# Kernel optimization log

Hardware: AMD Instinct MI355X
Metric: run time of the kernel (lower is better)

The kernel has to match this reference:

```python
import jax, jax.numpy as jnp
import numpy as np

BLOCK = 64
KH = 8        # num_k_head
G = 4         # gqa_group_size
D = 128       # model_hidden_size (head dim)
DG = 128      # gate_hidden_size
EPS = 1e-6
BSZ = 4
MAXS = 4096
LENGTHS = np.array([4096, 3584, 3072, 4096])


def rotate_half(x):
    h = x.shape[-1] // 2
    return jnp.concatenate([-x[..., h:], x[..., :h]], axis=-1)


def rmsnorm(x, w):
    x32 = x.astype(jnp.float32)
    y = x32 * jax.lax.rsqrt(jnp.mean(x32 * x32, axis=-1, keepdims=True) + EPS)
    return (y * w).astype(x.dtype)


def _rope_tables(n_pos, dim):
    inv = 1.0 / (10000.0 ** (np.arange(0, dim, 2, dtype=np.float32) / dim))
    ang = np.arange(n_pos, dtype=np.float32)[:, None] * inv[None, :]
    emb = np.concatenate([ang, ang], axis=-1)
    return np.cos(emb), np.sin(emb)


def setup_inputs() -> dict:
    key = jax.random.key(0)
    k1, k2, k3, k4, k5, k6 = jax.random.split(key, 6)
    total = int(LENGTHS.sum())
    cu = np.concatenate([[0], np.cumsum(LENGTHS)]).astype(np.int32)
    unpad_idx = np.concatenate([b * MAXS + np.arange(L) for b, L in enumerate(LENGTHS)]).astype(np.int64)
    # block-causal + validity mask (bool), shape (BSZ, 1, MAXS, MAXS//BLOCK)
    nb = MAXS // BLOCK
    qpos = np.arange(MAXS)
    bidx = np.arange(nb)
    causal = (qpos[:, None] // BLOCK) >= bidx[None, :]
    qvalid = qpos[None, :] < LENGTHS[:, None]
    bvalid = (bidx * BLOCK)[None, :] < LENGTHS[:, None]
    mask = causal[None] & qvalid[:, :, None] & bvalid[:, None, :]
    cos_q, sin_q = _rope_tables(MAXS, DG)
    cos_k, sin_k = _rope_tables(nb, DG)
    xavq = float(np.sqrt(6.0 / (D + DG)))
    xavk = float(np.sqrt(6.0 / (2 * D + DG)))
    return {
        "q": jax.random.normal(k1, (total, KH * G, D), jnp.float32),
        "k": jax.random.normal(k2, (total, KH, D), jnp.float32),
        "wq": jax.random.uniform(k3, (KH, G, D, DG), jnp.float32, -xavq, xavq),
        "wk": jax.random.uniform(k4, (KH, 2 * D, DG), jnp.float32, -xavk, xavk),
        "qnorm_w": jnp.ones((DG,), jnp.float32),
        "knorm_w": jnp.ones((DG,), jnp.float32),
        "cos_q": jnp.tile(jnp.asarray(cos_q)[None], (BSZ, 1, 1)),
        "sin_q": jnp.tile(jnp.asarray(sin_q)[None], (BSZ, 1, 1)),
        "cos_k": jnp.tile(jnp.asarray(cos_k)[None], (BSZ, 1, 1)),
        "sin_k": jnp.tile(jnp.asarray(sin_k)[None], (BSZ, 1, 1)),
        "attention_mask": jnp.asarray(mask)[:, None, :, :],
        "cu_seqlens": jnp.asarray(cu),
        "unpad_indices": jnp.asarray(unpad_idx),
        "max_seqlen": MAXS,
    }


def reference(q, k, wq, wk, qnorm_w, knorm_w, cos_q, sin_q, cos_k, sin_k,
              attention_mask, cu_seqlens, unpad_indices, max_seqlen):
    T = q.shape[0]
    bsz = cu_seqlens.shape[0] - 1
    nb = max_seqlen // BLOCK
    lengths = cu_seqlens[1:] - cu_seqlens[:-1]

    # --- Q path: per-group head-pooling projection (HeadPoolingLinear, Qproj) ---
    qp = jnp.einsum('skgi,kgio->sko', q.reshape(T, KH, G, D), wq)  # (T, KH, DG)
    qpad = jnp.zeros((bsz * max_seqlen, KH, DG), q.dtype).at[unpad_indices].set(qp)
    qpad = qpad.reshape(bsz, max_seqlen, KH, DG).transpose(0, 2, 1, 3)  # (b, KH, S, DG)
    qpad = rmsnorm(qpad, qnorm_w)
    qpad = qpad * cos_q[:, None] + rotate_half(qpad) * sin_q[:, None]

    # --- K path: pad, block max+avg pool (masked for varlen), project ---
    kpad = jnp.zeros((bsz * max_seqlen, KH, D), k.dtype).at[unpad_indices].set(k)
    kpad = kpad.reshape(bsz, nb, BLOCK, KH, D)
    pos = jnp.arange(max_seqlen).reshape(nb, BLOCK)
    valid = pos[None] < lengths[:, None, None]          # (b, nb, BLOCK)
    v = valid[..., None, None]                          # (b, nb, BLOCK, 1, 1)
    cnt = valid.sum(-1)[..., None, None]                # (b, nb, 1, 1)
    kmax = jnp.where(v, kpad, -jnp.inf).max(axis=2)
    kmax = jnp.where(cnt > 0, kmax, 0.0)
    kavg = jnp.where(v, kpad, 0.0).sum(axis=2) / jnp.maximum(cnt, 1).astype(k.dtype)
    kcat = jnp.concatenate([kmax, kavg], axis=-1)       # (b, nb, KH, 2D)
    kk = jnp.einsum('bhsi,hio->bhso', kcat.transpose(0, 2, 1, 3), wk)  # (b, KH, nb, DG)
    kk = rmsnorm(kk, knorm_w)
    kk = kk * cos_k[:, None] + rotate_half(kk) * sin_k[:, None]

    # --- QK gate scores ---
    attn = jnp.einsum('bhsd,bhtd->bhst', qpad, kk) * (1.0 / np.sqrt(DG))
    return jnp.where(attention_mask, attn, -1e20)
```

## Files before the change

kernel.cpp:

```cpp
#include <hip/hip_runtime.h>
#include <cstdint>
#include <cstddef>

#define BSZ   4
#define MAXS  4096
#define NB    64
#define KH    8
#define DH    128
#define DG    128
#define KHGD  4096
#define GD    512

typedef __attribute__((ext_vector_type(8))) short  short8;
typedef __attribute__((ext_vector_type(4))) float  f32x4;

static __device__ __forceinline__ unsigned bf16hi_bits(float x) {
    unsigned u = __float_as_uint(x);
    return (u + 0x7FFFu + ((u >> 16) & 1u)) & 0xFFFF0000u;
}
static __device__ __forceinline__ unsigned short bf16_rne(float x) {
    unsigned u = __float_as_uint(x);
    return (unsigned short)((u + 0x7FFFu + ((u >> 16) & 1u)) >> 16);
}

__global__ __launch_bounds__(256)
void prep_wq(const float* __restrict__ wq, unsigned short* __restrict__ Bp)
{
    const int wid  = blockIdx.x * 4 + (threadIdx.x >> 6);
    const int lane = threadIdx.x & 63;
    const int h  = wid >> 7, kt = (wid >> 4) & 7, kf = (wid >> 3) & 1, cf = wid & 7;
    const int n  = cf * 16 + (lane & 15);
    const int k0 = kt * 64 + kf * 32 + (lane >> 4) * 8;

    short8 hi, lo;
#pragma unroll
    for (int j = 0; j < 8; ++j) {
        const float x = wq[(size_t)(h * GD + k0 + j) * DG + n];
        const unsigned hb = bf16hi_bits(x);
        hi[j] = (short)(hb >> 16);
        lo[j] = (short)bf16_rne(x - __uint_as_float(hb));
    }
    unsigned short* p = Bp + (size_t)wid * 1024 + lane * 8;
    *(short8*)p         = hi;
    *(short8*)(p + 512) = lo;
}

__global__ __launch_bounds__(64, 2)
void qproj_mfma(const float* __restrict__ q,
                const unsigned short* __restrict__ Bp,
                const float* __restrict__ qnw,
                const float* __restrict__ cosq,
                const float* __restrict__ sinq,
                const int*   __restrict__ cu,
                unsigned short* __restrict__ qh,
                unsigned short* __restrict__ ql,
                int T)
{
    const int lane = threadIdx.x;
    const int h    = blockIdx.x;
    const int row0 = blockIdx.y * 64;
    const int lr = lane & 15, lq = lane >> 4;

    f32x4 acc[4][8];
#pragma unroll
    for (int rf = 0; rf < 4; ++rf)
#pragma unroll
        for (int cf = 0; cf < 8; ++cf) acc[rf][cf] = (f32x4){0.f, 0.f, 0.f, 0.f};

    const float* qb = q + (size_t)h * GD + lq * 8;
    const float* aptr[4];
#pragma unroll
    for (int rf = 0; rf < 4; ++rf) {
        int grow = row0 + rf * 16 + lr;
        if (grow > T - 1) grow = T - 1;
        aptr[rf] = qb + (size_t)grow * KHGD;
    }

    for (int kt = 0; kt < 8; ++kt) {
        const int kb = kt * 64;
#pragma unroll
        for (int kf = 0; kf < 2; ++kf) {
            f32x4 a0[4], a1[4];
#pragma unroll
            for (int rf = 0; rf < 4; ++rf) {
                const float* p = aptr[rf] + kb + kf * 32;
                a0[rf] = *(const f32x4*)p;
                a1[rf] = *(const f32x4*)(p + 4);
            }
            short8 ah[4], al[4];
#pragma unroll
            for (int rf = 0; rf < 4; ++rf) {
#pragma unroll
                for (int j = 0; j < 4; ++j) {
                    float x = a0[rf][j];
                    unsigned hb = bf16hi_bits(x);
                    ah[rf][j] = (short)(hb >> 16);
                    al[rf][j] = (short)bf16_rne(x - __uint_as_float(hb));
                    float y = a1[rf][j];
                    unsigned hb2 = bf16hi_bits(y);
                    ah[rf][j + 4] = (short)(hb2 >> 16);
                    al[rf][j + 4] = (short)bf16_rne(y - __uint_as_float(hb2));
                }
            }
            const unsigned short* bp =
                Bp + (size_t)(((h * 8 + kt) * 2 + kf) * 8) * 1024 + lane * 8;
#pragma unroll
            for (int cf = 0; cf < 8; ++cf) {
                const short8 bh = *(const short8*)(bp + cf * 1024);
                const short8 bl = *(const short8*)(bp + cf * 1024 + 512);
#pragma unroll
                for (int rf = 0; rf < 4; ++rf) {
                    acc[rf][cf] = __builtin_amdgcn_mfma_f32_16x16x32_bf16(ah[rf], bh, acc[rf][cf], 0, 0, 0);
                    acc[rf][cf] = __builtin_amdgcn_mfma_f32_16x16x32_bf16(ah[rf], bl, acc[rf][cf], 0, 0, 0);
                    acc[rf][cf] = __builtin_amdgcn_mfma_f32_16x16x32_bf16(al[rf], bh, acc[rf][cf], 0, 0, 0);
                }
            }
        }
    }

    const int cu1 = cu[1], cu2 = cu[2], cu3 = cu[3];
    float wn[8];
#pragma unroll
    for (int cf = 0; cf < 8; ++cf) wn[cf] = qnw[cf * 16 + lr];

#pragma unroll
    for (int rf = 0; rf < 4; ++rf) {
#pragma unroll
        for (int r = 0; r < 4; ++r) {
            float vv[8];
            float ss = 0.f;
#pragma unroll
            for (int cf = 0; cf < 8; ++cf) { vv[cf] = acc[rf][cf][r]; ss += vv[cf] * vv[cf]; }
            ss += __shfl_xor(ss, 1);
            ss += __shfl_xor(ss, 2);
            ss += __shfl_xor(ss, 4);
            ss += __shfl_xor(ss, 8);
            const float rn = 1.0f / sqrtf(ss * (1.0f / 128.0f) + 1e-6f);

            const int t = row0 + rf * 16 + lq * 4 + r;
            if (t < T) {
                int b = 0, cub = 0;
                if (t >= cu1) { b = 1; cub = cu1; }
                if (t >= cu2) { b = 2; cub = cu2; }
                if (t >= cu3) { b = 3; cub = cu3; }
                const int s = t - cub;

                float y[8];
#pragma unroll
                for (int cf = 0; cf < 8; ++cf) y[cf] = vv[cf] * rn * wn[cf];

                const float* cb = cosq + ((size_t)b * MAXS + s) * DG + lr;
                const float* sb = sinq + ((size_t)b * MAXS + s) * DG + lr;
                unsigned short* oh = qh + ((size_t)t * KH + h) * DG + lr;
                unsigned short* ol = ql + ((size_t)t * KH + h) * DG + lr;
#pragma unroll
                for (int cf = 0; cf < 8; ++cf) {
                    const float rot = (cf < 4) ? -y[cf + 4] : y[cf - 4];
                    const float o = y[cf] * cb[cf * 16] + rot * sb[cf * 16];
                    const unsigned hb = bf16hi_bits(o);
                    oh[cf * 16] = (unsigned short)(hb >> 16);
                    ol[cf * 16] = bf16_rne(o - __uint_as_float(hb));
                }
            }
        }
    }
}

__global__ __launch_bounds__(256, 2)
void kproj_kernel(const float* __restrict__ k,
                  const float* __restrict__ wk,
                  const float* __restrict__ knw,
                  const float* __restrict__ cosk,
                  const float* __restrict__ sink,
                  const int*   __restrict__ cu,
                  unsigned short* __restrict__ krh,
                  unsigned short* __restrict__ krl)
{
    __shared__ float kcat[KH][2 * DH];

    const int tid = threadIdx.x;
    const int blk = blockIdx.x, b = blockIdx.y;
    const int lb = cu[b];
    const int L  = cu[b + 1] - lb;
    const int nv = min(64, L - blk * 64);
    if (nv <= 0) return;

    const float* kbase = k + (size_t)(lb + blk * 64) * (KH * DH) + tid * 4;
    float4 vmax = make_float4(-3.0e38f, -3.0e38f, -3.0e38f, -3.0e38f);
    float4 vsum = make_float4(0.f, 0.f, 0.f, 0.f);
#pragma unroll 4
    for (int j = 0; j < nv; ++j) {
        const float4 v = *(const float4*)(kbase + (size_t)j * (KH * DH));
        vmax.x = fmaxf(vmax.x, v.x); vmax.y = fmaxf(vmax.y, v.y);
        vmax.z = fmaxf(vmax.z, v.z); vmax.w = fmaxf(vmax.w, v.w);
        vsum.x += v.x; vsum.y += v.y; vsum.z += v.z; vsum.w += v.w;
    }
    {
        const float inv = 1.0f / (float)nv;
        const int hh = tid >> 5, dd = (tid & 31) * 4;
        *(float4*)&kcat[hh][dd] = vmax;
        const float4 va = make_float4(vsum.x * inv, vsum.y * inv, vsum.z * inv, vsum.w * inv);
        *(float4*)&kcat[hh][128 + dd] = va;
    }
    __syncthreads();

    const int h = tid >> 5, oc = tid & 31, o = oc * 4;
    float4 a4 = make_float4(0.f, 0.f, 0.f, 0.f);
    const float* wbb = wk + (size_t)h * (2 * DH) * DG + o;
#pragma unroll 8
    for (int kk = 0; kk < 2 * DH; ++kk) {
        const float a = kcat[h][kk];
        const float4 w = *(const float4*)(wbb + (size_t)kk * DG);
        a4.x += a * w.x; a4.y += a * w.y; a4.z += a * w.z; a4.w += a * w.w;
    }

    float ss = a4.x * a4.x + a4.y * a4.y + a4.z * a4.z + a4.w * a4.w;
    ss += __shfl_xor(ss, 1);
    ss += __shfl_xor(ss, 2);
    ss += __shfl_xor(ss, 4);
    ss += __shfl_xor(ss, 8);
    ss += __shfl_xor(ss, 16);
    const float r = 1.0f / sqrtf(ss * (1.0f / 128.0f) + 1e-6f);

    const float4 wn = *(const float4*)(knw + o);
    const float y0 = a4.x * r * wn.x;
    const float y1 = a4.y * r * wn.y;
    const float y2 = a4.z * r * wn.z;
    const float y3 = a4.w * r * wn.w;

    const float p0 = __shfl_xor(y0, 16);
    const float p1 = __shfl_xor(y1, 16);
    const float p2 = __shfl_xor(y2, 16);
    const float p3 = __shfl_xor(y3, 16);
    const float r0 = (oc < 16) ? -p0 : p0;
    const float r1 = (oc < 16) ? -p1 : p1;
    const float r2 = (oc < 16) ? -p2 : p2;
    const float r3 = (oc < 16) ? -p3 : p3;

    const float* cb = cosk + ((size_t)b * NB + blk) * DG + o;
    const float* sb = sink + ((size_t)b * NB + blk) * DG + o;
    const float4 c4 = *(const float4*)cb;
    const float4 s4 = *(const float4*)sb;

    float v[4];
    v[0] = y0 * c4.x + r0 * s4.x;
    v[1] = y1 * c4.y + r1 * s4.y;
    v[2] = y2 * c4.z + r2 * s4.z;
    v[3] = y3 * c4.w + r3 * s4.w;

    ushort4 sh, sl;
    unsigned hb;
    hb = bf16hi_bits(v[0]); sh.x = (unsigned short)(hb >> 16); sl.x = bf16_rne(v[0] - __uint_as_float(hb));
    hb = bf16hi_bits(v[1]); sh.y = (unsigned short)(hb >> 16); sl.y = bf16_rne(v[1] - __uint_as_float(hb));
    hb = bf16hi_bits(v[2]); sh.z = (unsigned short)(hb >> 16); sl.z = bf16_rne(v[2] - __uint_as_float(hb));
    hb = bf16hi_bits(v[3]); sh.w = (unsigned short)(hb >> 16); sl.w = bf16_rne(v[3] - __uint_as_float(hb));

    const size_t ko = (((size_t)b * KH + h) * NB + blk) * DG + o;
    *(ushort4*)(krh + ko) = sh;
    *(ushort4*)(krl + ko) = sl;
}

__global__ __launch_bounds__(256, 2)
void score_mfma(const unsigned short* __restrict__ qh,
                const unsigned short* __restrict__ ql,
                const unsigned short* __restrict__ krh,
                const unsigned short* __restrict__ krl,
                const int* __restrict__ cu,
                float* __restrict__ out, int T)
{
    const int tid = threadIdx.x;
    const int lane = tid & 63, wid = tid >> 6;
    const int c = blockIdx.x, h = blockIdx.y, b = blockIdx.z;
    const int L = cu[b + 1] - cu[b];
    float* ob = out + (((size_t)b * KH + h) * MAXS + c * 64) * NB;

    if (c * 64 >= L) {
        const f32x4 m4 = (f32x4){-1e20f, -1e20f, -1e20f, -1e20f};
#pragma unroll
        for (int i = 0; i < 4; ++i) ((f32x4*)ob)[tid + i * 256] = m4;
        return;
    }
    const int nt  = c + 1;
    const int ncf = (nt + 15) >> 4;
    const int lr = lane & 15, lq = lane >> 4;

    int qrow = cu[b] + c * 64 + wid * 16 + lr;
    if (qrow > T - 1) qrow = T - 1;
    const unsigned short* qhp = qh + ((size_t)qrow * KH + h) * DG + lq * 8;
    const unsigned short* qlp = ql + ((size_t)qrow * KH + h) * DG + lq * 8;
    const unsigned short* kbh = krh + (((size_t)b * KH + h) * NB + lr) * DG + lq * 8;
    const unsigned short* kbl = krl + (((size_t)b * KH + h) * NB + lr) * DG + lq * 8;

    f32x4 acc[4];
#pragma unroll
    for (int cf = 0; cf < 4; ++cf) acc[cf] = (f32x4){0.f, 0.f, 0.f, 0.f};

#pragma unroll
    for (int kf = 0; kf < 4; ++kf) {
        const short8 ah = *(const short8*)(qhp + kf * 32);
        const short8 al = *(const short8*)(qlp + kf * 32);
#pragma unroll
        for (int cf = 0; cf < 4; ++cf) {
            if (cf < ncf) {
                const short8 bh = *(const short8*)(kbh + cf * 2048 + kf * 32);
                const short8 bl = *(const short8*)(kbl + cf * 2048 + kf * 32);
                acc[cf] = __builtin_amdgcn_mfma_f32_16x16x32_bf16(ah, bh, acc[cf], 0, 0, 0);
                acc[cf] = __builtin_amdgcn_mfma_f32_16x16x32_bf16(ah, bl, acc[cf], 0, 0, 0);
                acc[cf] = __builtin_amdgcn_mfma_f32_16x16x32_bf16(al, bh, acc[cf], 0, 0, 0);
            }
        }
    }

    const float scale = 0.08838834764831845f;
#pragma unroll
    for (int cf = 0; cf < 4; ++cf) {
        const int t = cf * 16 + lr;
#pragma unroll
        for (int r = 0; r < 4; ++r) {
            const int srow = c * 64 + wid * 16 + lq * 4 + r;
            float v = (cf < ncf) ? acc[cf][r] * scale : -1e20f;
            v = (srow < L && t < nt) ? v : -1e20f;
            ob[(size_t)(wid * 16 + lq * 4 + r) * NB + t] = v;
        }
    }
}

extern "C" void kernel_launch(void* const* d_in, const int* in_sizes, int n_in,
                              void* d_out, int out_size, void* d_ws, size_t ws_size,
                              hipStream_t stream)
{
    const float* q    = (const float*)d_in[0];
    const float* k    = (const float*)d_in[1];
    const float* wq   = (const float*)d_in[2];
    const float* wk   = (const float*)d_in[3];
    const float* qnw  = (const float*)d_in[4];
    const float* knw  = (const float*)d_in[5];
    const float* cosq = (const float*)d_in[6];
    const float* sinq = (const float*)d_in[7];
    const float* cosk = (const float*)d_in[8];
    const float* sink = (const float*)d_in[9];
    const int*   cu   = (const int*)d_in[11];

    const int T = in_sizes[0] / KHGD;

    unsigned short* qh  = (unsigned short*)d_ws;
    unsigned short* ql  = qh  + (size_t)T * KH * DG;
    unsigned short* krh = ql  + (size_t)T * KH * DG;
    unsigned short* krl = krh + (size_t)BSZ * KH * NB * DG;
    unsigned short* Bp  = krl + (size_t)BSZ * KH * NB * DG;
    (void)ws_size; (void)n_in; (void)out_size;

    prep_wq<<<256, 256, 0, stream>>>(wq, Bp);
    kproj_kernel<<<dim3(NB, BSZ), 256, 0, stream>>>(k, wk, knw, cosk, sink, cu, krh, krl);
    qproj_mfma<<<dim3(KH, (T + 63) / 64), 64, 0, stream>>>(q, Bp, qnw, cosq, sinq, cu, qh, ql, T);
    score_mfma<<<dim3(NB, KH, BSZ), 256, 0, stream>>>(qh, ql, krh, krl, cu, (float*)d_out, T);
}
```

Measured before the change: 513.7 us.

## Fuse Q projection with gate score computation, staging rotated Q in LDS

Merges the Q projection/RMSNorm/RoPE kernel and the QK score kernel into one kernel per (batch, 64-row chunk, head). The normalized, rotated Q tile is staged through swizzled shared memory instead of being written to and re-read from global hi/lo bf16 buffers. This removes that intermediate global traffic and one launch. It also swaps MFMA operand roles so weights are the A operand, and uses truncation rather than round-to-nearest for the bf16 hi/lo split, which slightly changes numerics.

After: 516.0 us. Within noise of the previous version (+0.5%).

```diff
diff --git a/kernel.cpp b/kernel.cpp
--- a/kernel.cpp
+++ b/kernel.cpp
@@ -11,8 +11,12 @@
 #define KHGD  4096
 #define GD    512
 
-typedef __attribute__((ext_vector_type(8))) short  short8;
-typedef __attribute__((ext_vector_type(4))) float  f32x4;
+typedef __attribute__((ext_vector_type(8))) short        short8;
+typedef __attribute__((ext_vector_type(4))) float        f32x4;
+typedef __attribute__((ext_vector_type(4))) unsigned int u32x4;
+typedef __attribute__((ext_vector_type(2))) unsigned int u32x2;
+
+union frag16 { u32x4 u; short8 s; };
 
 static __device__ __forceinline__ unsigned bf16hi_bits(float x) {
     unsigned u = __float_as_uint(x);
@@ -21,6 +25,15 @@
 static __device__ __forceinline__ unsigned short bf16_rne(float x) {
     unsigned u = __float_as_uint(x);
     return (unsigned short)((u + 0x7FFFu + ((u >> 16) & 1u)) >> 16);
+}
+static __device__ __forceinline__ void split_pair(float x0, float x1,
+                                                  unsigned& hi, unsigned& lo) {
+    unsigned u0 = __float_as_uint(x0), u1 = __float_as_uint(x1);
+    unsigned h0 = u0 & 0xFFFF0000u, h1 = u1 & 0xFFFF0000u;
+    float r0 = x0 - __uint_as_float(h0);
+    float r1 = x1 - __uint_as_float(h1);
+    hi = (u0 >> 16) | h1;
+    lo = (__float_as_uint(r0) >> 16) | (__float_as_uint(r1) & 0xFFFF0000u);
 }
 
 __global__ __launch_bounds__(256)
@@ -28,9 +41,9 @@
 {
     const int wid  = blockIdx.x * 4 + (threadIdx.x >> 6);
     const int lane = threadIdx.x & 63;
-    const int h  = wid >> 7, kt = (wid >> 4) & 7, kf = (wid >> 3) & 1, cf = wid & 7;
-    const int n  = cf * 16 + (lane & 15);
-    const int k0 = kt * 64 + kf * 32 + (lane >> 4) * 8;
+    const int h  = wid >> 7, kf16 = (wid >> 3) & 15, of = wid & 7;
+    const int n  = of * 16 + (lane & 15);
+    const int k0 = kf16 * 32 + (lane >> 4) * 8;
 
     short8 hi, lo;
 #pragma unroll
@@ -43,127 +56,6 @@
     unsigned short* p = Bp + (size_t)wid * 1024 + lane * 8;
     *(short8*)p         = hi;
     *(short8*)(p + 512) = lo;
-}
-
-__global__ __launch_bounds__(64, 2)
-void qproj_mfma(const float* __restrict__ q,
-                const unsigned short* __restrict__ Bp,
-                const float* __restrict__ qnw,
-                const float* __restrict__ cosq,
-                const float* __restrict__ sinq,
-                const int*   __restrict__ cu,
-                unsigned short* __restrict__ qh,
-                unsigned short* __restrict__ ql,
-                int T)
-{
-    const int lane = threadIdx.x;
-    const int h    = blockIdx.x;
-    const int row0 = blockIdx.y * 64;
-    const int lr = lane & 15, lq = lane >> 4;
-
-    f32x4 acc[4][8];
-#pragma unroll
-    for (int rf = 0; rf < 4; ++rf)
-#pragma unroll
-        for (int cf = 0; cf < 8; ++cf) acc[rf][cf] = (f32x4){0.f, 0.f, 0.f, 0.f};
-
-    const float* qb = q + (size_t)h * GD + lq * 8;
-    const float* aptr[4];
-#pragma unroll
-    for (int rf = 0; rf < 4; ++rf) {
-        int grow = row0 + rf * 16 + lr;
-        if (grow > T - 1) grow = T - 1;
-        aptr[rf] = qb + (size_t)grow * KHGD;
-    }
-
-    for (int kt = 0; kt < 8; ++kt) {
-        const int kb = kt * 64;
-#pragma unroll
-        for (int kf = 0; kf < 2; ++kf) {
-            f32x4 a0[4], a1[4];
-#pragma unroll
-            for (int rf = 0; rf < 4; ++rf) {
-                const float* p = aptr[rf] + kb + kf * 32;
-                a0[rf] = *(const f32x4*)p;
-                a1[rf] = *(const f32x4*)(p + 4);
-            }
-            short8 ah[4], al[4];
-#pragma unroll
-            for (int rf = 0; rf < 4; ++rf) {
-#pragma unroll
-                for (int j = 0; j < 4; ++j) {
-                    float x = a0[rf][j];
-                    unsigned hb = bf16hi_bits(x);
-                    ah[rf][j] = (short)(hb >> 16);
-                    al[rf][j] = (short)bf16_rne(x - __uint_as_float(hb));
-                    float y = a1[rf][j];
-                    unsigned hb2 = bf16hi_bits(y);
-                    ah[rf][j + 4] = (short)(hb2 >> 16);
-                    al[rf][j + 4] = (short)bf16_rne(y - __uint_as_float(hb2));
-                }
-            }
-            const unsigned short* bp =
-                Bp + (size_t)(((h * 8 + kt) * 2 + kf) * 8) * 1024 + lane * 8;
-#pragma unroll
-            for (int cf = 0; cf < 8; ++cf) {
-                const short8 bh = *(const short8*)(bp + cf * 1024);
-                const short8 bl = *(const short8*)(bp + cf * 1024 + 512);
-#pragma unroll
-                for (int rf = 0; rf < 4; ++rf) {
-                    acc[rf][cf] = __builtin_amdgcn_mfma_f32_16x16x32_bf16(ah[rf], bh, acc[rf][cf], 0, 0, 0);
-                    acc[rf][cf] = __builtin_amdgcn_mfma_f32_16x16x32_bf16(ah[rf], bl, acc[rf][cf], 0, 0, 0);
-                    acc[rf][cf] = __builtin_amdgcn_mfma_f32_16x16x32_bf16(al[rf], bh, acc[rf][cf], 0, 0, 0);
-                }
-            }
-        }
-    }
-
-    const int cu1 = cu[1], cu2 = cu[2], cu3 = cu[3];
-    float wn[8];
-#pragma unroll
-    for (int cf = 0; cf < 8; ++cf) wn[cf] = qnw[cf * 16 + lr];
-
-#pragma unroll
-    for (int rf = 0; rf < 4; ++rf) {
-#pragma unroll
-        for (int r = 0; r < 4; ++r) {
-            float vv[8];
-            float ss = 0.f;
-#pragma unroll
-            for (int cf = 0; cf < 8; ++cf) { vv[cf] = acc[rf][cf][r]; ss += vv[cf] * vv[cf]; }
-            ss += __shfl_xor(ss, 1);
-            ss += __shfl_xor(ss, 2);
-            ss += __shfl_xor(ss, 4);
-            ss += __shfl_xor(ss, 8);
-            const float rn = 1.0f / sqrtf(ss * (1.0f / 128.0f) + 1e-6f);
-
-            const int t = row0 + rf * 16 + lq * 4 + r;
-            if (t < T) {
-                int b = 0, cub = 0;
-                if (t >= cu1) { b = 1; cub = cu1; }
-                if (t >= cu2) { b = 2; cub = cu2; }
-                if (t >= cu3) { b = 3; cub = cu3; }
-                const int s = t - cub;
-
-                float y[8];
-#pragma unroll
-                for (int cf = 0; cf < 8; ++cf) y[cf] = vv[cf] * rn * wn[cf];
-
-                const float* cb = cosq + ((size_t)b * MAXS + s) * DG + lr;
-                const float* sb = sinq + ((size_t)b * MAXS + s) * DG + lr;
-                unsigned short* oh = qh + ((size_t)t * KH + h) * DG + lr;
-                unsigned short* ol = ql + ((size_t)t * KH + h) * DG + lr;
-#pragma unroll
-                for (int cf = 0; cf < 8; ++cf) {
-                    const float rot = (cf < 4) ? -y[cf + 4] : y[cf - 4];
-                    const float o = y[cf] * cb[cf * 16] + rot * sb[cf * 16];
-                    const unsigned hb = bf16hi_bits(o);
-                    oh[cf * 16] = (unsigned short)(hb >> 16);
-                    ol[cf * 16] = bf16_rne(o - __uint_as_float(hb));
-                }
-            }
-        }
-    }
 }
 
 __global__ __launch_bounds__(256, 2)
@@ -260,67 +152,159 @@
     *(ushort4*)(krl + ko) = sl;
 }
 
-__global__ __launch_bounds__(256, 2)
-void score_mfma(const unsigned short* __restrict__ qh,
-                const unsigned short* __restrict__ ql,
-                const unsigned short* __restrict__ krh,
-                const unsigned short* __restrict__ krl,
-                const int* __restrict__ cu,
-                float* __restrict__ out, int T)
+__global__ __launch_bounds__(64, 2)
+void qscore_fused(const float* __restrict__ q,
+                  const unsigned short* __restrict__ Bp,
+                  const float* __restrict__ qnw,
+                  const float* __restrict__ cosq,
+                  const float* __restrict__ sinq,
+                  const unsigned short* __restrict__ krh,
+                  const unsigned short* __restrict__ krl,
+                  const int* __restrict__ cu,
+                  float* __restrict__ out)
 {
-    const int tid = threadIdx.x;
-    const int lane = tid & 63, wid = tid >> 6;
-    const int c = blockIdx.x, h = blockIdx.y, b = blockIdx.z;
-    const int L = cu[b + 1] - cu[b];
+    __shared__ unsigned short ldsh[2048];
+    __shared__ unsigned short ldsl[2048];
+
+    const int lane = threadIdx.x;
+    const int lq = lane >> 4, lr = lane & 15;
+    const int h = blockIdx.y;
+    const int b = blockIdx.x >> 6, c = blockIdx.x & 63;
+    const int lb = cu[b];
+    const int L  = cu[b + 1] - lb;
     float* ob = out + (((size_t)b * KH + h) * MAXS + c * 64) * NB;
 
     if (c * 64 >= L) {
-        const f32x4 m4 = (f32x4){-1e20f, -1e20f, -1e20f, -1e20f};
-#pragma unroll
-        for (int i = 0; i < 4; ++i) ((f32x4*)ob)[tid + i * 256] = m4;
+        const f32x4 m4 = {-1e20f, -1e20f, -1e20f, -1e20f};
+#pragma unroll
+        for (int i = 0; i < 16; ++i) ((f32x4*)ob)[lane + i * 64] = m4;
         return;
     }
+
+    f32x4 acc[8][4];
+#pragma unroll
+    for (int of = 0; of < 8; ++of)
+#pragma unroll
+        for (int sf = 0; sf < 4; ++sf) acc[of][sf] = (f32x4){0.f, 0.f, 0.f, 0.f};
+
+    const float* qbase = q + (size_t)(lb + c * 64) * KHGD + h * GD;
+    const unsigned short* bpb = Bp + (size_t)h * 16 * 8192 + lane * 8;
+
+#pragma unroll 2
+    for (int kf = 0; kf < 16; ++kf) {
+        frag16 bh[4], bl[4];
+#pragma unroll
+        for (int sf = 0; sf < 4; ++sf) {
+            const float* p = qbase + (size_t)(sf * 16 + lr) * KHGD + kf * 32 + lq * 8;
+            const f32x4 x0 = *(const f32x4*)p;
+            const f32x4 x1 = *(const f32x4*)(p + 4);
+            unsigned hw0, lw0, hw1, lw1, hw2, lw2, hw3, lw3;
+            split_pair(x0[0], x0[1], hw0, lw0);
+            split_pair(x0[2], x0[3], hw1, lw1);
+            split_pair(x1[0], x1[1], hw2, lw2);
+            split_pair(x1[2], x1[3], hw3, lw3);
+            bh[sf].u = (u32x4){hw0, hw1, hw2, hw3};
+            bl[sf].u = (u32x4){lw0, lw1, lw2, lw3};
+        }
+        const unsigned short* bpk = bpb + (size_t)kf * 8192;
+#pragma unroll
+        for (int of = 0; of < 8; ++of) {
+            const short8 ah = *(const short8*)(bpk + of * 1024);
+            const short8 al = *(const short8*)(bpk + of * 1024 + 512);
+#pragma unroll
+            for (int sf = 0; sf < 4; ++sf) {
+                acc[of][sf] = __builtin_amdgcn_mfma_f32_16x16x32_bf16(ah, bh[sf].s, acc[of][sf], 0, 0, 0);
+                acc[of][sf] = __builtin_amdgcn_mfma_f32_16x16x32_bf16(ah, bl[sf].s, acc[of][sf], 0, 0, 0);
+                acc[of][sf] = __builtin_amdgcn_mfma_f32_16x16x32_bf16(al, bh[sf].s, acc[of][sf], 0, 0, 0);
+            }
+        }
+    }
+
+    f32x4 wn4[8];
+#pragma unroll
+    for (int of = 0; of < 8; ++of)
+        wn4[of] = *(const f32x4*)(qnw + of * 16 + lq * 4);
+
     const int nt  = c + 1;
     const int ncf = (nt + 15) >> 4;
-    const int lr = lane & 15, lq = lane >> 4;
-
-    int qrow = cu[b] + c * 64 + wid * 16 + lr;
-    if (qrow > T - 1) qrow = T - 1;
-    const unsigned short* qhp = qh + ((size_t)qrow * KH + h) * DG + lq * 8;
-    const unsigned short* qlp = ql + ((size_t)qrow * KH + h) * DG + lq * 8;
-    const unsigned short* kbh = krh + (((size_t)b * KH + h) * NB + lr) * DG + lq * 8;
-    const unsigned short* kbl = krl + (((size_t)b * KH + h) * NB + lr) * DG + lq * 8;
-
-    f32x4 acc[4];
-#pragma unroll
-    for (int cf = 0; cf < 4; ++cf) acc[cf] = (f32x4){0.f, 0.f, 0.f, 0.f};
-
-#pragma unroll
-    for (int kf = 0; kf < 4; ++kf) {
-        const short8 ah = *(const short8*)(qhp + kf * 32);
-        const short8 al = *(const short8*)(qlp + kf * 32);
+    const float scale = 0.08838834764831845f;
+    const unsigned short* krhb = krh + (((size_t)b * KH + h) * NB) * DG + lq * 8;
+    const unsigned short* krlb = krl + (((size_t)b * KH + h) * NB) * DG + lq * 8;
+
+#pragma unroll
+    for (int sf = 0; sf < 4; ++sf) {
+        float ss = 0.f;
+#pragma unroll
+        for (int of = 0; of < 8; ++of)
+#pragma unroll
+            for (int r = 0; r < 4; ++r) ss += acc[of][sf][r] * acc[of][sf][r];
+        ss += __shfl_xor(ss, 16);
+        ss += __shfl_xor(ss, 32);
+        const float rn = 1.0f / sqrtf(ss * (1.0f / 128.0f) + 1e-6f);
+
+        const int spos = c * 64 + sf * 16 + lr;
+        const float* cb = cosq + ((size_t)b * MAXS + spos) * DG + lq * 4;
+        const float* sb = sinq + ((size_t)b * MAXS + spos) * DG + lq * 4;
+
+        f32x4 y[8];
+#pragma unroll
+        for (int of = 0; of < 8; ++of)
+#pragma unroll
+            for (int r = 0; r < 4; ++r) y[of][r] = acc[of][sf][r] * rn * wn4[of][r];
+
+#pragma unroll
+        for (int of = 0; of < 8; ++of) {
+            const f32x4 cc = *(const f32x4*)(cb + of * 16);
+            const f32x4 sv = *(const f32x4*)(sb + of * 16);
+            f32x4 o4;
+#pragma unroll
+            for (int r = 0; r < 4; ++r) {
+                const float rot = (of < 4) ? -y[of + 4][r] : y[of - 4][r];
+                o4[r] = y[of][r] * cc[r] + rot * sv[r];
+            }
+            unsigned hw0, lw0, hw1, lw1;
+            split_pair(o4[0], o4[1], hw0, lw0);
+            split_pair(o4[2], o4[3], hw1, lw1);
+            int idx = lr * 128 + of * 16 + lq * 4;
+            idx ^= (lr & 7) << 3;
+            *(u32x2*)&ldsh[idx] = (u32x2){hw0, hw1};
+            *(u32x2*)&ldsl[idx] = (u32x2){lw0, lw1};
+        }
+
+        short8 qa_h[4], qa_l[4];
+#pragma unroll
+        for (int kf = 0; kf < 4; ++kf) {
+            int ridx = lr * 128 + kf * 32 + lq * 8;
+            ridx ^= (lr & 7) << 3;
+            qa_h[kf] = *(const short8*)&ldsh[ridx];
+            qa_l[kf] = *(const short8*)&ldsl[ridx];
+        }
+
+        f32x4 sacc[4];
+#pragma unroll
+        for (int cf = 0; cf < 4; ++cf) sacc[cf] = (f32x4){0.f, 0.f, 0.f, 0.f};
+        for (int cf = 0; cf < ncf; ++cf) {
+            const unsigned short* kh8p = krhb + (size_t)(cf * 16 + lr) * DG;
+            const unsigned short* kl8p = krlb + (size_t)(cf * 16 + lr) * DG;
+#pragma unroll
+            for (int kf = 0; kf < 4; ++kf) {
+                const short8 kh8 = *(const short8*)(kh8p + kf * 32);
+                const short8 kl8 = *(const short8*)(kl8p + kf * 32);
+                sacc[cf] = __builtin_amdgcn_mfma_f32_16x16x32_bf16(qa_h[kf], kh8, sacc[cf], 0, 0, 0);
+                sacc[cf] = __builtin_amdgcn_mfma_f32_16x16x32_bf16(qa_l[kf], kh8, sacc[cf], 0, 0, 0);
+                sacc[cf] = __builtin_amdgcn_mfma_f32_16x16x32_bf16(qa_h[kf], kl8, sacc[cf], 0, 0, 0);
+            }
+        }
+
 #pragma unroll
         for (int cf = 0; cf < 4; ++cf) {
-            if (cf < ncf) {
-                const short8 bh = *(const short8*)(kbh + cf * 2048 + kf * 32);
-                const short8 bl = *(const short8*)(kbl + cf * 2048 + kf * 32);
-                acc[cf] = __builtin_amdgcn_mfma_f32_16x16x32_bf16(ah, bh, acc[cf], 0, 0, 0);
-                acc[cf] = __builtin_amdgcn_mfma_f32_16x16x32_bf16(ah, bl, acc[cf], 0, 0, 0);
-                acc[cf] = __builtin_amdgcn_mfma_f32_16x16x32_bf16(al, bh, acc[cf], 0, 0, 0);
+            const int t = cf * 16 + lr;
+            const bool tv = (t < nt);
+#pragma unroll
+            for (int r = 0; r < 4; ++r) {
+                const float v = tv ? sacc[cf][r] * scale : -1e20f;
+                ob[(size_t)(sf * 16 + lq * 4 + r) * NB + t] = v;
             }
-        }
-    }
-
-    const float scale = 0.08838834764831845f;
-#pragma unroll
-    for (int cf = 0; cf < 4; ++cf) {
-        const int t = cf * 16 + lr;
-#pragma unroll
-        for (int r = 0; r < 4; ++r) {
-            const int srow = c * 64 + wid * 16 + lq * 4 + r;
-            float v = (cf < ncf) ? acc[cf][r] * scale : -1e20f;
-            v = (srow < L && t < nt) ? v : -1e20f;
-            ob[(size_t)(wid * 16 + lq * 4 + r) * NB + t] = v;
         }
     }
 }
@@ -340,18 +324,13 @@
     const float* cosk = (const float*)d_in[8];
     const float* sink = (const float*)d_in[9];
     const int*   cu   = (const int*)d_in[11];
-
-    const int T = in_sizes[0] / KHGD;
-
-    unsigned short* qh  = (unsigned short*)d_ws;
-    unsigned short* ql  = qh  + (size_t)T * KH * DG;
-    unsigned short* krh = ql  + (size_t)T * KH * DG;
+    (void)in_sizes; (void)n_in; (void)out_size; (void)ws_size;
+
+    unsigned short* krh = (unsigned short*)d_ws;
     unsigned short* krl = krh + (size_t)BSZ * KH * NB * DG;
     unsigned short* Bp  = krl + (size_t)BSZ * KH * NB * DG;
-    (void)ws_size; (void)n_in; (void)out_size;
 
     prep_wq<<<256, 256, 0, stream>>>(wq, Bp);
     kproj_kernel<<<dim3(NB, BSZ), 256, 0, stream>>>(k, wk, knw, cosk, sink, cu, krh, krl);
-    qproj_mfma<<<dim3(KH, (T + 63) / 64), 64, 0, stream>>>(q, Bp, qnw, cosq, sinq, cu, qh, ql, T);
-    score_mfma<<<dim3(NB, KH, BSZ), 256, 0, stream>>>(qh, ql, krh, krl, cu, (float*)d_out, T);
-}
+    qscore_fused<<<dim3(BSZ * NB, KH), 64, 0, stream>>>(q, Bp, qnw, cosq, sinq, krh, krl, cu, (float*)d_out);
+}
```
